# Optimization experiments

Hardware: AMD Instinct MI355X
Metric: run time of the kernel (lower is better)

## Reference

```python
import jax, jax.numpy as jnp
import numpy as np

B = 16384
IN = 128
H = 128
NC = 10
NATT = 3
EPS = 1e-5


def setup_inputs() -> dict:
    key = jax.random.key(0)
    ks = jax.random.split(key, 8)
    s_in = 1.0 / np.sqrt(IN)
    s_h = 1.0 / np.sqrt(H)
    return {
        "x": jax.random.normal(ks[0], (B, IN), dtype=jnp.float32),
        "W_in": jax.random.uniform(ks[1], (IN, H), jnp.float32, -s_in, s_in),
        "b_in": jax.random.uniform(ks[2], (H,), jnp.float32, -s_in, s_in),
        "W_att": jax.random.uniform(ks[3], (NATT, H, H), jnp.float32, -s_h, s_h),
        "b_att": jax.random.uniform(ks[4], (NATT, H), jnp.float32, -s_h, s_h),
        "gamma": jnp.ones((NATT, H), jnp.float32),
        "beta": jnp.zeros((NATT, H), jnp.float32),
        "W_c": jax.random.uniform(ks[5], (H, NC), jnp.float32, -s_h, s_h),
        "b_c": jax.random.uniform(ks[6], (NC,), jnp.float32, -s_h, s_h),
    }


def _layernorm(y, g, b):
    mu = jnp.mean(y, axis=-1, keepdims=True)
    var = jnp.mean((y - mu) ** 2, axis=-1, keepdims=True)
    return (y - mu) * jax.lax.rsqrt(var + EPS) * g + b


def reference(x, W_in, b_in, W_att, b_att, gamma, beta, W_c, b_c):
    # in_proj: [B, IN] -> [B, H]
    h = x @ W_in + b_in
    for i in range(NATT):
        u = jnp.tanh(h @ W_att[i] + b_att[i])            # [B, H]
        scores = u[:, :, None] * u[:, None, :]            # outer product [B, H, H]
        attn = jax.nn.softmax(scores, axis=-1)
        out = jnp.einsum("bij,bj->bi", attn, h)          # [B, H]
        h = _layernorm(h + out, gamma[i], beta[i])
    return h @ W_c + b_c                                  # [B, NC]
```

## Files before the change

### kernel.cpp

```cpp
#include <hip/hip_runtime.h>
#include <math.h>

#define B_TOT 16384
#define H     128
#define NC    10
#define NATT  3
#define TR    16
#define HBS   136
#define KT    5
#define EPS   1e-5f

typedef __attribute__((ext_vector_type(8))) short bf16x8;
typedef __attribute__((ext_vector_type(4))) float f32x4;

__device__ __forceinline__ ushort f2bf(float f) {
    union { float f; unsigned u; } v; v.f = f;
    unsigned r = v.u + 0x7fffu + ((v.u >> 16) & 1u);
    return (ushort)(r >> 16);
}

__device__ __forceinline__ float fast_tanh(float a) {
    float t = __expf(2.f * a);
    return 1.f - 2.f * __builtin_amdgcn_rcpf(t + 1.f);
}

template<int CTRL>
__device__ __forceinline__ float dpp_add(float v) {
    int x = __float_as_int(v);
    int y = __builtin_amdgcn_update_dpp(0, x, CTRL, 0xf, 0xf, false);
    return v + __int_as_float(y);
}
__device__ __forceinline__ float red16(float v) {
    v = dpp_add<0x121>(v);
    v = dpp_add<0x122>(v);
    v = dpp_add<0x124>(v);
    v = dpp_add<0x128>(v);
    return v;
}

extern "C" __global__ __launch_bounds__(256)
void prep_weights(const float* __restrict__ W_in,
                  const float* __restrict__ W_att,
                  const float* __restrict__ W_c,
                  ushort* __restrict__ wt)
{
    int i = blockIdx.x * 256 + threadIdx.x;
    if (i < 65536) {
        int mat = i >> 14, idx = i & 16383;
        int k = idx >> 7, n = idx & 127;
        float v = (mat == 0) ? W_in[idx] : W_att[(mat - 1) * 16384 + idx];
        wt[mat * 16384 + n * H + k] = f2bf(v);
    } else if (i < 65536 + 2048) {
        int idx = i - 65536;
        int n = idx >> 7, k = idx & 127;
        float v = (n < NC) ? W_c[k * NC + n] : 0.f;
        wt[65536 + n * H + k] = f2bf(v);
    }
}

extern "C" __global__ __launch_bounds__(256, 4)
void simple_attention_kernel(const float* __restrict__ x,
                             const float* __restrict__ b_in,
                             const float* __restrict__ b_att,
                             const float* __restrict__ gamma,
                             const float* __restrict__ beta,
                             const float* __restrict__ b_c,
                             const ushort* __restrict__ wt,
                             float* __restrict__ out)
{
    __shared__ __align__(16) ushort ab[TR * HBS];
    __shared__ __align__(16) float  exm[4 * 16 * 12];
    __shared__ __align__(16) float  exl[4 * 16 * 2];

    const int tid  = threadIdx.x;
    const int wv   = tid >> 6;
    const int lane = tid & 63;
    const int s    = lane & 15;
    const int q    = lane >> 4;
    const size_t rowBase = (size_t)blockIdx.x * TR;

    float h[2][4];
    f32x4 acc[2];

    {
        const float* xp = x + (rowBase + s) * H + 32 * wv + q * 8;
        float4 v0 = *(const float4*)xp;
        float4 v1 = *(const float4*)(xp + 4);
        bf16x8 a;
        a[0] = f2bf(v0.x); a[1] = f2bf(v0.y); a[2] = f2bf(v0.z); a[3] = f2bf(v0.w);
        a[4] = f2bf(v1.x); a[5] = f2bf(v1.y); a[6] = f2bf(v1.z); a[7] = f2bf(v1.w);
        *(bf16x8*)&ab[s * HBS + 32 * wv + q * 8] = a;
    }
    __syncthreads();

    {
        bf16x8 af[4];
        #pragma unroll
        for (int ks = 0; ks < 4; ++ks)
            af[ks] = *(const bf16x8*)&ab[s * HBS + ks * 32 + q * 8];
        #pragma unroll
        for (int t = 0; t < 2; ++t) acc[t] = (f32x4){0.f, 0.f, 0.f, 0.f};
        #pragma unroll
        for (int ks = 0; ks < 4; ++ks) {
            #pragma unroll
            for (int t = 0; t < 2; ++t) {
                bf16x8 b = *(const bf16x8*)&wt[(32 * wv + 16 * t + s) * H + ks * 32 + q * 8];
                acc[t] = __builtin_amdgcn_mfma_f32_16x16x32_bf16(af[ks], b, acc[t], 0, 0, 0);
            }
        }
        __syncthreads();
        #pragma unroll
        for (int t = 0; t < 2; ++t) {
            int n = 32 * wv + 16 * t + s;
            float bi = b_in[n];
            #pragma unroll
            for (int r = 0; r < 4; ++r) {
                h[t][r] = acc[t][r] + bi;
                ab[(4 * q + r) * HBS + n] = f2bf(h[t][r]);
            }
        }
        __syncthreads();
    }

    const float cm[KT] = {1.00004478f, 0.99730768f, 0.49919676f, 0.17734736f, 0.04379392f};

    #pragma unroll 1
    for (int layer = 0; layer < NATT; ++layer) {
        const ushort* WT = wt + (size_t)(1 + layer) * 16384;

        bf16x8 af[4];
        #pragma unroll
        for (int ks = 0; ks < 4; ++ks)
            af[ks] = *(const bf16x8*)&ab[s * HBS + ks * 32 + q * 8];
        #pragma unroll
        for (int t = 0; t < 2; ++t) acc[t] = (f32x4){0.f, 0.f, 0.f, 0.f};
        #pragma unroll
        for (int ks = 0; ks < 4; ++ks) {
            #pragma unroll
            for (int t = 0; t < 2; ++t) {
                bf16x8 b = *(const bf16x8*)&WT[(32 * wv + 16 * t + s) * H + ks * 32 + q * 8];
                acc[t] = __builtin_amdgcn_mfma_f32_16x16x32_bf16(af[ks], b, acc[t], 0, 0, 0);
            }
        }
        float u[2][4];
        #pragma unroll
        for (int t = 0; t < 2; ++t) {
            float ba = b_att[layer * H + 32 * wv + 16 * t + s];
            #pragma unroll
            for (int r = 0; r < 4; ++r) u[t][r] = fast_tanh(acc[t][r] + ba);
        }

        float S[4][KT], T[4][KT - 1];
        #pragma unroll
        for (int r = 0; r < 4; ++r) {
            #pragma unroll
            for (int k = 0; k < KT; ++k) S[r][k] = 0.f;
            #pragma unroll
            for (int k = 0; k < KT - 1; ++k) T[r][k] = 0.f;
        }
        #pragma unroll
        for (int t = 0; t < 2; ++t) {
            #pragma unroll
            for (int r = 0; r < 4; ++r) {
                float uu = u[t][r], hh = h[t][r];
                S[r][0] += hh;
                float p = uu;
                S[r][1] += p * hh; T[r][0] += p;
                #pragma unroll
                for (int k = 2; k < KT; ++k) {
                    p *= uu;
                    S[r][k] += p * hh;
                    T[r][k - 1] += p;
                }
            }
        }
        #pragma unroll
        for (int r = 0; r < 4; ++r) {
            #pragma unroll
            for (int k = 0; k < KT; ++k)     S[r][k] = red16(S[r][k]);
            #pragma unroll
            for (int k = 0; k < KT - 1; ++k) T[r][k] = red16(T[r][k]);
        }
        if (s == 0) {
            #pragma unroll
            for (int r = 0; r < 4; ++r) {
                float* dst = &exm[(wv * 16 + 4 * q + r) * 12];
                *(f32x4*)&dst[0] = (f32x4){S[r][0], S[r][1], S[r][2], S[r][3]};
                *(f32x4*)&dst[4] = (f32x4){S[r][4], T[r][0], T[r][1], T[r][2]};
                dst[8] = T[r][3];
            }
        }
        __syncthreads();
        #pragma unroll
        for (int r = 0; r < 4; ++r) {
            f32x4 s0 = (f32x4){0.f, 0.f, 0.f, 0.f};
            f32x4 s1 = (f32x4){0.f, 0.f, 0.f, 0.f};
            float s2 = 0.f;
            #pragma unroll
            for (int ow = 0; ow < 4; ++ow) {
                const float* src = &exm[(ow * 16 + 4 * q + r) * 12];
                s0 += *(const f32x4*)&src[0];
                s1 += *(const f32x4*)&src[4];
                s2 += src[8];
            }
            S[r][0] = s0.x * cm[0];
            S[r][1] = s0.y * cm[1];
            S[r][2] = s0.z * cm[2];
            S[r][3] = s0.w * cm[3];
            S[r][4] = s1.x * cm[4];
            T[r][0] = s1.y * cm[1];
            T[r][1] = s1.z * cm[2];
            T[r][2] = s1.w * cm[3];
            T[r][3] = s2   * cm[4];
        }

        float ls[4] = {0, 0, 0, 0}, lq[4] = {0, 0, 0, 0};
        #pragma unroll
        for (int t = 0; t < 2; ++t) {
            #pragma unroll
            for (int r = 0; r < 4; ++r) {
                float uu = u[t][r];
                float num = S[r][KT - 1];
                #pragma unroll
                for (int k = KT - 2; k >= 0; --k) num = num * uu + S[r][k];
                float den = T[r][KT - 2];
                #pragma unroll
                for (int k = KT - 3; k >= 0; --k) den = den * uu + T[r][k];
                den = den * uu + 128.f * 1.00004478f;
                float yy = h[t][r] + num * __builtin_amdgcn_rcpf(den);
                h[t][r] = yy;
                ls[r] += yy; lq[r] += yy * yy;
            }
        }
        #pragma unroll
        for (int r = 0; r < 4; ++r) { ls[r] = red16(ls[r]); lq[r] = red16(lq[r]); }
        if (s == 0) {
            #pragma unroll
            for (int r = 0; r < 4; ++r)
                *(float2*)&exl[(wv * 16 + 4 * q + r) * 2] = make_float2(ls[r], lq[r]);
        }
        __syncthreads();
        float mu[4], inv[4];
        #pragma unroll
        for (int r = 0; r < 4; ++r) {
            float sm = 0.f, sq = 0.f;
            #pragma unroll
            for (int ow = 0; ow < 4; ++ow) {
                float2 o = *(const float2*)&exl[(ow * 16 + 4 * q + r) * 2];
                sm += o.x; sq += o.y;
            }
            mu[r] = sm * (1.f / H);
            float var = sq * (1.f / H) - mu[r] * mu[r];
            inv[r] = rsqrtf(var + EPS);
        }
        #pragma unroll
        for (int t = 0; t < 2; ++t) {
            int n = 32 * wv + 16 * t + s;
            float g  = gamma[layer * H + n];
            float be = beta [layer * H + n];
            #pragma unroll
            for (int r = 0; r < 4; ++r) {
                float hn = (h[t][r] - mu[r]) * inv[r] * g + be;
                h[t][r] = hn;
                ab[(4 * q + r) * HBS + n] = f2bf(hn);
            }
        }
        __syncthreads();
    }

    if (wv == 0) {
        const ushort* WC = wt + 4 * 16384;
        f32x4 facc = (f32x4){0.f, 0.f, 0.f, 0.f};
        #pragma unroll
        for (int ks = 0; ks < 4; ++ks) {
            bf16x8 a = *(const bf16x8*)&ab[s * HBS + ks * 32 + q * 8];
            bf16x8 b = *(const bf16x8*)&WC[s * H + ks * 32 + q * 8];
            facc = __builtin_amdgcn_mfma_f32_16x16x32_bf16(a, b, facc, 0, 0, 0);
        }
        if (s < NC) {
            float bc = b_c[s];
            #pragma unroll
            for (int r = 0; r < 4; ++r)
                out[(rowBase + 4 * q + r) * NC + s] = facc[r] + bc;
        }
    }
}

extern "C" void kernel_launch(void* const* d_in, const int* in_sizes, int n_in,
                              void* d_out, int out_size, void* d_ws, size_t ws_size,
                              hipStream_t stream) {
    const float* x     = (const float*)d_in[0];
    const float* W_in  = (const float*)d_in[1];
    const float* b_in  = (const float*)d_in[2];
    const float* W_att = (const float*)d_in[3];
    const float* b_att = (const float*)d_in[4];
    const float* gamma = (const float*)d_in[5];
    const float* beta  = (const float*)d_in[6];
    const float* W_c   = (const float*)d_in[7];
    const float* b_c   = (const float*)d_in[8];
    float* out  = (float*)d_out;
    ushort* wt  = (ushort*)d_ws;

    hipLaunchKernelGGL(prep_weights, dim3(264), dim3(256), 0, stream,
                       W_in, W_att, W_c, wt);
    hipLaunchKernelGGL(simple_attention_kernel, dim3(B_TOT / TR), dim3(256), 0, stream,
                       x, b_in, b_att, gamma, beta, b_c, wt, out);
}
```

Baseline: 104.6 us.

## Fold LayerNorm affine into next layer's weights and defer normalization

Folds the previous layer's LayerNorm gamma into the attention weight matrix and gamma/beta into precomputed bias vectors, so the un-normalized pre-LN activation is fed directly to the next matmul and normalization is applied after it. This removes one __syncthreads per intermediate layer and overlaps the LN statistic exchange with the matmul. It also replaces the four-way cross-wave shared-memory sum with a strided layout plus a 4-lane DPP reduction. The cost is extra aux vectors, serial 128-long dot loops in the prep kernel, and bf16 rounding of unnormalized activations, which may change accuracy.

```diff
diff --git a/kernel.cpp b/kernel.cpp
--- a/kernel.cpp
+++ b/kernel.cpp
@@ -9,6 +9,8 @@
 #define HBS   136
 #define KT    5
 #define EPS   1e-5f
+#define EXM_CS 196
+#define EXL_CS 34
 
 typedef __attribute__((ext_vector_type(8))) short bf16x8;
 typedef __attribute__((ext_vector_type(4))) float f32x4;
@@ -37,11 +39,19 @@
     v = dpp_add<0x128>(v);
     return v;
 }
+__device__ __forceinline__ float red4ror(float v) {
+    v = dpp_add<0x121>(v);
+    v = dpp_add<0x122>(v);
+    return v;
+}
 
 extern "C" __global__ __launch_bounds__(256)
 void prep_weights(const float* __restrict__ W_in,
                   const float* __restrict__ W_att,
                   const float* __restrict__ W_c,
+                  const float* __restrict__ gamma,
+                  const float* __restrict__ beta,
+                  const float* __restrict__ b_att,
                   ushort* __restrict__ wt)
 {
     int i = blockIdx.x * 256 + threadIdx.x;
@@ -49,19 +59,45 @@
         int mat = i >> 14, idx = i & 16383;
         int k = idx >> 7, n = idx & 127;
         float v = (mat == 0) ? W_in[idx] : W_att[(mat - 1) * 16384 + idx];
+        if (mat >= 2) v *= gamma[(mat - 2) * H + k];
         wt[mat * 16384 + n * H + k] = f2bf(v);
     } else if (i < 65536 + 2048) {
         int idx = i - 65536;
         int n = idx >> 7, k = idx & 127;
         float v = (n < NC) ? W_c[k * NC + n] : 0.f;
         wt[65536 + n * H + k] = f2bf(v);
+    } else if (i < 67584 + 1536) {
+        int j = i - 67584;
+        int l = j >> 9;
+        int idx = j & 511;
+        int g = idx >> 7;
+        int n = idx & 127;
+        float* aux = (float*)(wt + 67584);
+        float v;
+        if (g == 0) {
+            v = 0.f;
+            if (l > 0) {
+                for (int k = 0; k < H; ++k)
+                    v += gamma[(l - 1) * H + k] * W_att[l * 16384 + k * H + n];
+            }
+        } else if (g == 1) {
+            v = b_att[l * H + n];
+            if (l > 0) {
+                for (int k = 0; k < H; ++k)
+                    v += beta[(l - 1) * H + k] * W_att[l * 16384 + k * H + n];
+            }
+        } else if (g == 2) {
+            v = (l == 0) ? 1.f : gamma[(l - 1) * H + n];
+        } else {
+            v = (l == 0) ? 0.f : beta[(l - 1) * H + n];
+        }
+        aux[l * 512 + g * 128 + n] = v;
     }
 }
 
 extern "C" __global__ __launch_bounds__(256, 4)
 void simple_attention_kernel(const float* __restrict__ x,
                              const float* __restrict__ b_in,
-                             const float* __restrict__ b_att,
                              const float* __restrict__ gamma,
                              const float* __restrict__ beta,
                              const float* __restrict__ b_c,
@@ -69,8 +105,8 @@
                              float* __restrict__ out)
 {
     __shared__ __align__(16) ushort ab[TR * HBS];
-    __shared__ __align__(16) float  exm[4 * 16 * 12];
-    __shared__ __align__(16) float  exl[4 * 16 * 2];
+    __shared__ __align__(16) float  exm[4 * EXM_CS];
+    __shared__ __align__(16) float  exl[4 * EXL_CS];
 
     const int tid  = threadIdx.x;
     const int wv   = tid >> 6;
@@ -78,8 +114,9 @@
     const int s    = lane & 15;
     const int q    = lane >> 4;
     const size_t rowBase = (size_t)blockIdx.x * TR;
-
-    float h[2][4];
+    const float* aux = (const float*)(wt + 67584);
+
+    float y[2][4];
     f32x4 acc[2];
 
     {
@@ -115,8 +152,8 @@
             float bi = b_in[n];
             #pragma unroll
             for (int r = 0; r < 4; ++r) {
-                h[t][r] = acc[t][r] + bi;
-                ab[(4 * q + r) * HBS + n] = f2bf(h[t][r]);
+                y[t][r] = acc[t][r] + bi;
+                ab[(4 * q + r) * HBS + n] = f2bf(y[t][r]);
             }
         }
         __syncthreads();
@@ -127,6 +164,7 @@
     #pragma unroll 1
     for (int layer = 0; layer < NATT; ++layer) {
         const ushort* WT = wt + (size_t)(1 + layer) * 16384;
+        const float* AX  = aux + layer * 512;
 
         bf16x8 af[4];
         #pragma unroll
@@ -142,12 +180,38 @@
                 acc[t] = __builtin_amdgcn_mfma_f32_16x16x32_bf16(af[ks], b, acc[t], 0, 0, 0);
             }
         }
+
+        float mu[4], inv[4], invmu[4];
+        if (layer == 0) {
+            #pragma unroll
+            for (int r = 0; r < 4; ++r) { mu[r] = 0.f; inv[r] = 1.f; invmu[r] = 0.f; }
+        } else {
+            #pragma unroll
+            for (int r = 0; r < 4; ++r) {
+                float2 o = *(const float2*)&exl[(s & 3) * EXL_CS + (4 * q + r) * 2];
+                float sm = red4ror(o.x), sq = red4ror(o.y);
+                mu[r] = sm * (1.f / H);
+                float var = sq * (1.f / H) - mu[r] * mu[r];
+                inv[r] = rsqrtf(var + EPS);
+                invmu[r] = inv[r] * mu[r];
+            }
+        }
+
         float u[2][4];
         #pragma unroll
         for (int t = 0; t < 2; ++t) {
-            float ba = b_att[layer * H + 32 * wv + 16 * t + s];
-            #pragma unroll
-            for (int r = 0; r < 4; ++r) u[t][r] = fast_tanh(acc[t][r] + ba);
+            int n = 32 * wv + 16 * t + s;
+            float gwv = AX[n];
+            float c1v = AX[128 + n];
+            float gpv = AX[256 + n];
+            float bpv = AX[384 + n];
+            #pragma unroll
+            for (int r = 0; r < 4; ++r) {
+                float pre = fmaf(inv[r], acc[t][r], fmaf(-invmu[r], gwv, c1v));
+                u[t][r] = fast_tanh(pre);
+                float hN = fmaf((y[t][r] - mu[r]) * inv[r], gpv, bpv);
+                y[t][r] = hN;
+            }
         }
 
         float S[4][KT], T[4][KT - 1];
@@ -162,7 +226,7 @@
         for (int t = 0; t < 2; ++t) {
             #pragma unroll
             for (int r = 0; r < 4; ++r) {
-                float uu = u[t][r], hh = h[t][r];
+                float uu = u[t][r], hh = y[t][r];
                 S[r][0] += hh;
                 float p = uu;
                 S[r][1] += p * hh; T[r][0] += p;
@@ -184,7 +248,7 @@
         if (s == 0) {
             #pragma unroll
             for (int r = 0; r < 4; ++r) {
-                float* dst = &exm[(wv * 16 + 4 * q + r) * 12];
+                float* dst = &exm[wv * EXM_CS + (4 * q + r) * 12];
                 *(f32x4*)&dst[0] = (f32x4){S[r][0], S[r][1], S[r][2], S[r][3]};
                 *(f32x4*)&dst[4] = (f32x4){S[r][4], T[r][0], T[r][1], T[r][2]};
                 dst[8] = T[r][3];
@@ -193,25 +257,19 @@
         __syncthreads();
         #pragma unroll
         for (int r = 0; r < 4; ++r) {
-            f32x4 s0 = (f32x4){0.f, 0.f, 0.f, 0.f};
-            f32x4 s1 = (f32x4){0.f, 0.f, 0.f, 0.f};
-            float s2 = 0.f;
-            #pragma unroll
-            for (int ow = 0; ow < 4; ++ow) {
-                const float* src = &exm[(ow * 16 + 4 * q + r) * 12];
-                s0 += *(const f32x4*)&src[0];
-                s1 += *(const f32x4*)&src[4];
-                s2 += src[8];
-            }
-            S[r][0] = s0.x * cm[0];
-            S[r][1] = s0.y * cm[1];
-            S[r][2] = s0.z * cm[2];
-            S[r][3] = s0.w * cm[3];
-            S[r][4] = s1.x * cm[4];
-            T[r][0] = s1.y * cm[1];
-            T[r][1] = s1.z * cm[2];
-            T[r][2] = s1.w * cm[3];
-            T[r][3] = s2   * cm[4];
+            const float* src = &exm[(s & 3) * EXM_CS + (4 * q + r) * 12];
+            f32x4 c0 = *(const f32x4*)&src[0];
+            f32x4 c1 = *(const f32x4*)&src[4];
+            float c2 = src[8];
+            S[r][0] = red4ror(c0.x) * cm[0];
+            S[r][1] = red4ror(c0.y) * cm[1];
+            S[r][2] = red4ror(c0.z) * cm[2];
+            S[r][3] = red4ror(c0.w) * cm[3];
+            S[r][4] = red4ror(c1.x) * cm[4];
+            T[r][0] = red4ror(c1.y) * cm[1];
+            T[r][1] = red4ror(c1.z) * cm[2];
+            T[r][2] = red4ror(c1.w) * cm[3];
+            T[r][3] = red4ror(c2)   * cm[4];
         }
 
         float ls[4] = {0, 0, 0, 0}, lq[4] = {0, 0, 0, 0};
@@ -227,45 +285,59 @@
                 #pragma unroll
                 for (int k = KT - 3; k >= 0; --k) den = den * uu + T[r][k];
                 den = den * uu + 128.f * 1.00004478f;
-                float yy = h[t][r] + num * __builtin_amdgcn_rcpf(den);
-                h[t][r] = yy;
+                float yy = y[t][r] + num * __builtin_amdgcn_rcpf(den);
+                y[t][r] = yy;
                 ls[r] += yy; lq[r] += yy * yy;
             }
         }
-        #pragma unroll
-        for (int r = 0; r < 4; ++r) { ls[r] = red16(ls[r]); lq[r] = red16(lq[r]); }
-        if (s == 0) {
-            #pragma unroll
-            for (int r = 0; r < 4; ++r)
-                *(float2*)&exl[(wv * 16 + 4 * q + r) * 2] = make_float2(ls[r], lq[r]);
-        }
-        __syncthreads();
-        float mu[4], inv[4];
-        #pragma unroll
-        for (int r = 0; r < 4; ++r) {
-            float sm = 0.f, sq = 0.f;
-            #pragma unroll
-            for (int ow = 0; ow < 4; ++ow) {
-                float2 o = *(const float2*)&exl[(ow * 16 + 4 * q + r) * 2];
-                sm += o.x; sq += o.y;
-            }
-            mu[r] = sm * (1.f / H);
-            float var = sq * (1.f / H) - mu[r] * mu[r];
-            inv[r] = rsqrtf(var + EPS);
-        }
-        #pragma unroll
-        for (int t = 0; t < 2; ++t) {
-            int n = 32 * wv + 16 * t + s;
-            float g  = gamma[layer * H + n];
-            float be = beta [layer * H + n];
-            #pragma unroll
-            for (int r = 0; r < 4; ++r) {
-                float hn = (h[t][r] - mu[r]) * inv[r] * g + be;
-                h[t][r] = hn;
-                ab[(4 * q + r) * HBS + n] = f2bf(hn);
-            }
-        }
-        __syncthreads();
+
+        if (layer < NATT - 1) {
+            #pragma unroll
+            for (int t = 0; t < 2; ++t) {
+                int n = 32 * wv + 16 * t + s;
+                #pragma unroll
+                for (int r = 0; r < 4; ++r)
+                    ab[(4 * q + r) * HBS + n] = f2bf(y[t][r]);
+            }
+            #pragma unroll
+            for (int r = 0; r < 4; ++r) { ls[r] = red16(ls[r]); lq[r] = red16(lq[r]); }
+            if (s == 0) {
+                #pragma unroll
+                for (int r = 0; r < 4; ++r)
+                    *(float2*)&exl[wv * EXL_CS + (4 * q + r) * 2] = make_float2(ls[r], lq[r]);
+            }
+            __syncthreads();
+        } else {
+            #pragma unroll
+            for (int r = 0; r < 4; ++r) { ls[r] = red16(ls[r]); lq[r] = red16(lq[r]); }
+            if (s == 0) {
+                #pragma unroll
+                for (int r = 0; r < 4; ++r)
+                    *(float2*)&exl[wv * EXL_CS + (4 * q + r) * 2] = make_float2(ls[r], lq[r]);
+            }
+            __syncthreads();
+            float mu2[4], inv2[4];
+            #pragma unroll
+            for (int r = 0; r < 4; ++r) {
+                float2 o = *(const float2*)&exl[(s & 3) * EXL_CS + (4 * q + r) * 2];
+                float sm = red4ror(o.x), sq = red4ror(o.y);
+                mu2[r] = sm * (1.f / H);
+                float var = sq * (1.f / H) - mu2[r] * mu2[r];
+                inv2[r] = rsqrtf(var + EPS);
+            }
+            #pragma unroll
+            for (int t = 0; t < 2; ++t) {
+                int n = 32 * wv + 16 * t + s;
+                float g  = gamma[layer * H + n];
+                float be = beta [layer * H + n];
+                #pragma unroll
+                for (int r = 0; r < 4; ++r) {
+                    float hn = (y[t][r] - mu2[r]) * inv2[r] * g + be;
+                    ab[(4 * q + r) * HBS + n] = f2bf(hn);
+                }
+            }
+            __syncthreads();
+        }
     }
 
     if (wv == 0) {
@@ -301,8 +373,8 @@
     float* out  = (float*)d_out;
     ushort* wt  = (ushort*)d_ws;
 
-    hipLaunchKernelGGL(prep_weights, dim3(264), dim3(256), 0, stream,
-                       W_in, W_att, W_c, wt);
+    hipLaunchKernelGGL(prep_weights, dim3(270), dim3(256), 0, stream,
+                       W_in, W_att, W_c, gamma, beta, b_att, wt);
     hipLaunchKernelGGL(simple_attention_kernel, dim3(B_TOT / TR), dim3(256), 0, stream,
-                       x, b_in, b_att, gamma, beta, b_c, wt, out);
-}
+                       x, b_in, gamma, beta, b_c, wt, out);
+}
```

Result: slower. 115.7 us (+10.6%).
